# Optimization experiments

Measured on AMD Instinct MI355X. Metric: run time of the kernel, lower is better.

## Reference

```python
import jax, jax.numpy as jnp
import numpy as np

HEADS = 8
DIM_HEAD = 64


def setup_inputs() -> dict:
    key = jax.random.key(0)
    k1, k2, k3 = jax.random.split(key, 3)
    dim_in = 256
    hidden = HEADS * DIM_HEAD  # 512
    x = jax.random.normal(k1, (2, dim_in, 64, 64), dtype=jnp.float32)
    # 1x1 conv weights stored as [out_ch, in_ch]
    w_qkv = jax.random.normal(k2, (3 * hidden, dim_in), dtype=jnp.float32) * (1.0 / np.sqrt(dim_in))
    w_out = jax.random.normal(k3, (dim_in, hidden), dtype=jnp.float32) * (1.0 / np.sqrt(hidden))
    b_out = jnp.zeros((dim_in,), dtype=jnp.float32)
    return {"x": x, "w_qkv": w_qkv, "w_out": w_out, "b_out": b_out}


def reference(x, w_qkv, w_out, b_out):
    b, c, H, W = x.shape
    S = H * W
    scale = 1.0 / np.sqrt(DIM_HEAD)
    # 1x1 conv == per-pixel linear projection
    qkv = jnp.einsum('bcxy,oc->boxy', x, w_qkv)  # [b, 3*hidden, H, W]
    q, k, v = jnp.split(qkv, 3, axis=1)
    # 'b (h c) x y -> b h c (x y)'
    def to_heads(z):
        return z.reshape(b, HEADS, DIM_HEAD, S)
    q = to_heads(q) * scale
    k = to_heads(k)
    v = to_heads(v)
    sim = jnp.einsum('bhdi,bhdj->bhij', q, k)  # [b, h, S, S]
    sim = sim - jax.lax.stop_gradient(jnp.max(sim, axis=-1, keepdims=True))
    attn = jax.nn.softmax(sim, axis=-1)
    out = jnp.einsum('bhij,bhdj->bhid', attn, v)  # [b, h, S, d]
    # 'b h (x y) d -> b (h d) x y'
    out = out.transpose(0, 1, 3, 2).reshape(b, HEADS * DIM_HEAD, H, W)
    return jnp.einsum('bcxy,oc->boxy', out, w_out) + b_out[None, :, None, None]
```

## Files before the change

kernel.cpp:

```cpp
#include <hip/hip_runtime.h>
#include <cmath>

#define S_TOT 4096
#define CIN   256
#define HID   512
#define NHEAD 8
#define DIMH  64

typedef __attribute__((ext_vector_type(8))) short bf16x8;
typedef __attribute__((ext_vector_type(4))) float f32x4;
typedef __attribute__((address_space(1))) const void gv_t;
typedef __attribute__((address_space(3))) void lv_t;

__device__ __forceinline__ ushort f2bf(float f) {
    union { float f; unsigned u; } v; v.f = f;
    unsigned r = (v.u + 0x7FFFu + ((v.u >> 16) & 1u)) >> 16;
    return (ushort)r;
}

__device__ __forceinline__ float exp2_fast(float x) {
    float r; asm("v_exp_f32 %0, %1" : "=v"(r) : "v"(x)); return r;
}

__device__ __forceinline__ unsigned cvt_pk_bf16(float lo, float hi) {
    unsigned r; asm("v_cvt_pk_bf16_f32 %0, %1, %2" : "=v"(r) : "v"(lo), "v"(hi)); return r;
}

#define QSCALE 0.18033688011112042f

__global__ __launch_bounds__(256)
void cast_f32_bf16(const float* __restrict__ in, ushort* __restrict__ out, long n) {
    long i = ((long)blockIdx.x * 256 + threadIdx.x) * 4;
    if (i < n) {
        float4 v = *(const float4*)&in[i];
        ushort4 p;
        p.x = f2bf(v.x); p.y = f2bf(v.y); p.z = f2bf(v.z); p.w = f2bf(v.w);
        *(ushort4*)&out[i] = p;
    }
}

__global__ __launch_bounds__(256)
void transpose_cast_x(const float* __restrict__ x, ushort* __restrict__ xt) {
    __shared__ float tb[64][65];
    const int t = threadIdx.x;
    const int s0 = blockIdx.x * 64, c0 = blockIdx.y * 64;
    const long xb = (long)blockIdx.z * CIN * S_TOT;
    #pragma unroll
    for (int i = 0; i < 16; ++i) {
        int idx = t + i * 256;
        int c = idx >> 6, s = idx & 63;
        tb[c][s] = x[xb + (long)(c0 + c) * S_TOT + s0 + s];
    }
    __syncthreads();
    const long ob = (long)blockIdx.z * S_TOT * CIN;
    const int s = t >> 2, cq = (t & 3) * 16;
    #pragma unroll
    for (int j = 0; j < 4; ++j) {
        ushort4 pk;
        pk.x = f2bf(tb[cq + j * 4 + 0][s]);
        pk.y = f2bf(tb[cq + j * 4 + 1][s]);
        pk.z = f2bf(tb[cq + j * 4 + 2][s]);
        pk.w = f2bf(tb[cq + j * 4 + 3][s]);
        *(ushort4*)&xt[ob + (long)(s0 + s) * CIN + c0 + cq + j * 4] = pk;
    }
}

template<int MODE>
__global__ __launch_bounds__(256)
void gemm_mfma_kernel(const ushort* __restrict__ Ag, const ushort* __restrict__ Bg,
                      void* __restrict__ outp, const float* __restrict__ bias,
                      int Kdim, long strideA, long strideB) {
    __shared__ __attribute__((aligned(16))) ushort Abuf[128 * 64];
    __shared__ __attribute__((aligned(16))) ushort Bbuf[128 * 64];
    const int t = threadIdx.x, lane = t & 63;
    const int l15 = lane & 15, g = lane >> 4;
    const int wid = t >> 6, wr = wid >> 1, wc = wid & 1;
    const int bz = blockIdx.z;
    const int am0 = blockIdx.y * 128, bn0 = blockIdx.x * 128;
    Ag += (long)bz * strideA;
    Bg += (long)bz * strideB;

    f32x4 acc[4][4];
    #pragma unroll
    for (int i = 0; i < 4; ++i)
        #pragma unroll
        for (int j = 0; j < 4; ++j)
            acc[i][j] = (f32x4){0.f, 0.f, 0.f, 0.f};

    for (int k0 = 0; k0 < Kdim; k0 += 64) {
        __syncthreads();
        #pragma unroll
        for (int i = 0; i < 4; ++i) {
            const int chunk = t + i * 256;
            const int row = chunk >> 3, sl = chunk & 7;
            const ushort* srcA = Ag + (long)(am0 + row) * Kdim + k0 + ((sl ^ (row & 7)) << 3);
            __builtin_amdgcn_global_load_lds((gv_t*)srcA,
                (lv_t*)((char*)Abuf + (i * 256 + (t & ~63)) * 16), 16, 0, 0);
            const ushort* srcB = Bg + (long)(bn0 + row) * Kdim + k0 + ((sl ^ (row & 7)) << 3);
            __builtin_amdgcn_global_load_lds((gv_t*)srcB,
                (lv_t*)((char*)Bbuf + (i * 256 + (t & ~63)) * 16), 16, 0, 0);
        }
        asm volatile("s_waitcnt vmcnt(0)" ::: "memory");
        __syncthreads();

        bf16x8 bfr[4][2];
        #pragma unroll
        for (int fn = 0; fn < 4; ++fn) {
            const int row = wc * 64 + fn * 16 + l15;
            #pragma unroll
            for (int hf = 0; hf < 2; ++hf)
                bfr[fn][hf] = *(const bf16x8*)((const char*)Bbuf + row * 128
                                + (((hf * 4 + g) ^ (row & 7)) << 4));
        }
        #pragma unroll
        for (int fm = 0; fm < 4; ++fm) {
            const int row = wr * 64 + fm * 16 + l15;
            const bf16x8 a0 = *(const bf16x8*)((const char*)Abuf + row * 128
                                + (((g) ^ (row & 7)) << 4));
            const bf16x8 a1 = *(const bf16x8*)((const char*)Abuf + row * 128
                                + (((4 + g) ^ (row & 7)) << 4));
            #pragma unroll
            for (int fn = 0; fn < 4; ++fn) {
                acc[fm][fn] = __builtin_amdgcn_mfma_f32_16x16x32_bf16(a0, bfr[fn][0], acc[fm][fn], 0, 0, 0);
                acc[fm][fn] = __builtin_amdgcn_mfma_f32_16x16x32_bf16(a1, bfr[fn][1], acc[fm][fn], 0, 0, 0);
            }
        }
    }

    #pragma unroll
    for (int fm = 0; fm < 4; ++fm)
        #pragma unroll
        for (int fn = 0; fn < 4; ++fn)
            #pragma unroll
            for (int r = 0; r < 4; ++r) {
                const int ar = am0 + wr * 64 + fm * 16 + g * 4 + r;
                const int bc = bn0 + wc * 64 + fn * 16 + l15;
                if (MODE == 0) {
                    const int which = bc >> 9, h = (bc >> 6) & 7, d = bc & 63;
                    const float scl = (which == 0) ? QSCALE : 1.0f;
                    ushort* O = (ushort*)outp;
                    O[(long)which * 4194304 + (((long)(bz * NHEAD + h)) * S_TOT + ar) * DIMH + d]
                        = f2bf(acc[fm][fn][r] * scl);
                } else if (MODE == 1) {
                    const int h = ar >> 6, d = ar & 63;
                    const int j = bc & 63;
                    const int pj = ((j >> 5) << 5) | (((j >> 2) & 3) << 3)
                                 | (((j >> 4) & 1) << 2) | (j & 3);
                    const int pc = (bc & ~63) | pj;
                    ushort* O = (ushort*)outp;
                    O[(((long)(bz * NHEAD + h)) * DIMH + d) * S_TOT + pc] = f2bf(acc[fm][fn][r]);
                } else {
                    float* O = (float*)outp;
                    O[((long)bz * CIN + ar) * S_TOT + bc] = acc[fm][fn][r] + bias[ar];
                }
            }
}

__global__ __launch_bounds__(512)
void attn_mfma_kernel(const ushort* __restrict__ qg, const ushort* __restrict__ kg,
                      const ushort* __restrict__ vg, ushort* __restrict__ aout) {
    __shared__ __attribute__((aligned(16))) ushort kbuf[2][64 * 64];
    __shared__ __attribute__((aligned(16))) ushort vbuf[2][64 * 64];

    const int t = threadIdx.x;
    const int lane = t & 63, wid = t >> 6;
    const int l15 = lane & 15, g = lane >> 4;
    const int h = blockIdx.y, b = blockIdx.z;
    const int bh = b * NHEAD + h;
    const int qrow0 = blockIdx.x * 128 + wid * 16;

    const ushort* qp = qg + ((long)bh * S_TOT + qrow0 + l15) * DIMH + g * 8;
    const bf16x8 qf0 = *(const bf16x8*)qp;
    const bf16x8 qf1 = *(const bf16x8*)(qp + 32);

    f32x4 oacc[4];
    #pragma unroll
    for (int f = 0; f < 4; ++f) oacc[f] = (f32x4){0.f, 0.f, 0.f, 0.f};
    float mrun = -3e38f, lrun = 0.f;

    const long kg_base = (long)bh * S_TOT * DIMH;
    const long vg_base = (long)bh * DIMH * S_TOT;
    const int sl = lane & 7, sr = lane >> 3;
    const int swz = sl ^ sr;

    auto STAGE = [&](int buf, long key0) {
        const int row = wid * 8 + sr;
        char* kdst = (char*)(&kbuf[buf][0]) + wid * 1024;
        char* vdst = (char*)(&vbuf[buf][0]) + wid * 1024;
        const char* srcK = (const char*)(kg + kg_base + (key0 + row) * DIMH) + swz * 16;
        __builtin_amdgcn_global_load_lds((gv_t*)srcK, (lv_t*)kdst, 16, 0, 0);
        const char* srcV = (const char*)(vg + vg_base + (long)row * S_TOT + key0) + swz * 16;
        __builtin_amdgcn_global_load_lds((gv_t*)srcV, (lv_t*)vdst, 16, 0, 0);
    };

    STAGE(0, 0);
    asm volatile("s_waitcnt vmcnt(0)" ::: "memory");
    __syncthreads();

    for (int kt0 = 0; kt0 < S_TOT / 64; ++kt0) {
        const int cur = kt0 & 1;
        if (kt0 + 1 < S_TOT / 64) STAGE(cur ^ 1, (long)(kt0 + 1) * 64);

        const char* kb_ = (const char*)(&kbuf[cur][0]);
        const char* vb_ = (const char*)(&vbuf[cur][0]);

        f32x4 sacc[4];
        __builtin_amdgcn_s_setprio(1);
        #pragma unroll
        for (int kb = 0; kb < 4; ++kb) {
            const int krow = kb * 16 + l15, ks = krow & 7;
            const bf16x8 kf0 = *(const bf16x8*)(kb_ + krow * 128 + ((g ^ ks) << 4));
            const bf16x8 kf1 = *(const bf16x8*)(kb_ + krow * 128 + (((4 + g) ^ ks) << 4));
            sacc[kb] = (f32x4){0.f, 0.f, 0.f, 0.f};
            sacc[kb] = __builtin_amdgcn_mfma_f32_16x16x32_bf16(kf0, qf0, sacc[kb], 0, 0, 0);
            sacc[kb] = __builtin_amdgcn_mfma_f32_16x16x32_bf16(kf1, qf1, sacc[kb], 0, 0, 0);
        }
        __builtin_amdgcn_s_setprio(0);

        float tmax = fmaxf(fmaxf(sacc[0][0], sacc[0][1]), fmaxf(sacc[0][2], sacc[0][3]));
        #pragma unroll
        for (int kb = 1; kb < 4; ++kb)
            tmax = fmaxf(tmax, fmaxf(fmaxf(sacc[kb][0], sacc[kb][1]),
                                     fmaxf(sacc[kb][2], sacc[kb][3])));

        if (__any(tmax > mrun + 8.0f)) {
            float tm = fmaxf(tmax, __shfl_xor(tmax, 16, 64));
            tm = fmaxf(tm, __shfl_xor(tm, 32, 64));
            const float mn = fmaxf(mrun, tm);
            const float al = exp2_fast(mrun - mn);
            lrun *= al;
            #pragma unroll
            for (int r = 0; r < 4; ++r) {
                const float alg = __shfl(al, g * 4 + r, 64);
                #pragma unroll
                for (int f = 0; f < 4; ++f) oacc[f][r] *= alg;
            }
            mrun = mn;
        }

        union { unsigned u[8]; bf16x8 v[2]; } pw;
        #pragma unroll
        for (int kb = 0; kb < 4; ++kb) {
            const float p0 = exp2_fast(sacc[kb][0] - mrun);
            const float p1 = exp2_fast(sacc[kb][1] - mrun);
            const float p2 = exp2_fast(sacc[kb][2] - mrun);
            const float p3 = exp2_fast(sacc[kb][3] - mrun);
            lrun += (p0 + p1) + (p2 + p3);
            pw.u[kb * 2]     = cvt_pk_bf16(p0, p1);
            pw.u[kb * 2 + 1] = cvt_pk_bf16(p2, p3);
        }

        __builtin_amdgcn_s_setprio(1);
        #pragma unroll
        for (int ks = 0; ks < 2; ++ks) {
            #pragma unroll
            for (int f = 0; f < 4; ++f) {
                const int vrow = f * 16 + l15;
                const bf16x8 vf = *(const bf16x8*)(vb_ + vrow * 128
                                    + (((ks * 4 + g) ^ (vrow & 7)) << 4));
                oacc[f] = __builtin_amdgcn_mfma_f32_16x16x32_bf16(pw.v[ks], vf, oacc[f], 0, 0, 0);
            }
        }
        __builtin_amdgcn_s_setprio(0);

        asm volatile("s_waitcnt vmcnt(0)" ::: "memory");
        __syncthreads();
    }

    lrun += __shfl_xor(lrun, 16, 64);
    lrun += __shfl_xor(lrun, 32, 64);
    #pragma unroll
    for (int r = 0; r < 4; ++r) {
        const float inv = 1.0f / __shfl(lrun, g * 4 + r, 64);
        const long srow = (long)b * S_TOT + qrow0 + g * 4 + r;
        #pragma unroll
        for (int f = 0; f < 4; ++f)
            aout[srow * HID + h * 64 + f * 16 + l15] = f2bf(oacc[f][r] * inv);
    }
}

extern "C" void kernel_launch(void* const* d_in, const int* in_sizes, int n_in,
                              void* d_out, int out_size, void* d_ws, size_t ws_size,
                              hipStream_t stream) {
    const float* x     = (const float*)d_in[0];
    const float* w_qkv = (const float*)d_in[1];
    const float* w_out = (const float*)d_in[2];
    const float* b_out = (const float*)d_in[3];
    float* out = (float*)d_out;

    const long PERQKV = (long)2 * NHEAD * S_TOT * DIMH;
    ushort* qws = (ushort*)d_ws;
    ushort* kws = qws + PERQKV;
    ushort* vws = kws + PERQKV;
    ushort* xt  = vws + PERQKV;
    ushort* wqb = xt + (long)2 * S_TOT * CIN;
    ushort* wob = wqb + (long)3 * HID * CIN;
    ushort* awb = wob + (long)CIN * HID;

    cast_f32_bf16<<<dim3((3 * HID * CIN / 4 + 255) / 256), 256, 0, stream>>>(
        w_qkv, wqb, (long)3 * HID * CIN);
    cast_f32_bf16<<<dim3((CIN * HID / 4 + 255) / 256), 256, 0, stream>>>(
        w_out, wob, (long)CIN * HID);
    transpose_cast_x<<<dim3(S_TOT / 64, CIN / 64, 2), 256, 0, stream>>>(x, xt);

    gemm_mfma_kernel<0><<<dim3(1024 / 128, S_TOT / 128, 2), 256, 0, stream>>>(
        xt, wqb, qws, nullptr, CIN, (long)S_TOT * CIN, 0L);
    gemm_mfma_kernel<1><<<dim3(S_TOT / 128, 512 / 128, 2), 256, 0, stream>>>(
        wqb + (long)1024 * CIN, xt, vws, nullptr, CIN, 0L, (long)S_TOT * CIN);

    attn_mfma_kernel<<<dim3(S_TOT / 128, NHEAD, 2), 512, 0, stream>>>(qws, kws, vws, awb);

    gemm_mfma_kernel<2><<<dim3(S_TOT / 128, CIN / 128, 2), 256, 0, stream>>>(
        wob, awb, out, b_out, HID, 0L, (long)S_TOT * HID);
}
```

Baseline: 135.0 us.

## Switch attention to 32x32x16 MFMA tiles with 32 query rows per wave

The attention kernel moves from 16x16x32 MFMA to 32x32x16 MFMA. Each wave now owns 32 query rows, and each block uses 4 waves of 256 threads with two blocks per CU. The running max is folded into the QK accumulator as a bias initialiser, which removes the per-element subtraction before exp. The P fragments are rearranged with cross-lane shuffles, so the V-layout permutation in the projection GEMM is dropped. The aim is fewer MFMA instructions and LDS reads per tile, paid for with more registers and extra shuffle traffic.

```diff
diff --git a/kernel.cpp b/kernel.cpp
--- a/kernel.cpp
+++ b/kernel.cpp
@@ -9,6 +9,7 @@
 
 typedef __attribute__((ext_vector_type(8))) short bf16x8;
 typedef __attribute__((ext_vector_type(4))) float f32x4;
+typedef __attribute__((ext_vector_type(16))) float f32x16;
 typedef __attribute__((address_space(1))) const void gv_t;
 typedef __attribute__((address_space(3))) void lv_t;
 
@@ -143,12 +144,8 @@
                         = f2bf(acc[fm][fn][r] * scl);
                 } else if (MODE == 1) {
                     const int h = ar >> 6, d = ar & 63;
-                    const int j = bc & 63;
-                    const int pj = ((j >> 5) << 5) | (((j >> 2) & 3) << 3)
-                                 | (((j >> 4) & 1) << 2) | (j & 3);
-                    const int pc = (bc & ~63) | pj;
                     ushort* O = (ushort*)outp;
-                    O[(((long)(bz * NHEAD + h)) * DIMH + d) * S_TOT + pc] = f2bf(acc[fm][fn][r]);
+                    O[(((long)(bz * NHEAD + h)) * DIMH + d) * S_TOT + bc] = f2bf(acc[fm][fn][r]);
                 } else {
                     float* O = (float*)outp;
                     O[((long)bz * CIN + ar) * S_TOT + bc] = acc[fm][fn][r] + bias[ar];
@@ -156,7 +153,34 @@
             }
 }
 
-__global__ __launch_bounds__(512)
+#define MKPF(SV, PFA, PFB) do {                                               \
+    const float e0 = exp2_fast(SV[0]),  e1 = exp2_fast(SV[1]);               \
+    const float e2 = exp2_fast(SV[2]),  e3 = exp2_fast(SV[3]);               \
+    const float e4 = exp2_fast(SV[4]),  e5 = exp2_fast(SV[5]);               \
+    const float e6 = exp2_fast(SV[6]),  e7 = exp2_fast(SV[7]);               \
+    const float e8 = exp2_fast(SV[8]),  e9 = exp2_fast(SV[9]);               \
+    const float ea = exp2_fast(SV[10]), eb = exp2_fast(SV[11]);              \
+    const float ec = exp2_fast(SV[12]), ed = exp2_fast(SV[13]);              \
+    const float ee = exp2_fast(SV[14]), ef = exp2_fast(SV[15]);              \
+    lrun += (((e0+e1)+(e2+e3)) + ((e4+e5)+(e6+e7)))                          \
+          + (((e8+e9)+(ea+eb)) + ((ec+ed)+(ee+ef)));                         \
+    const unsigned x0 = cvt_pk_bf16(e0,e1), x1 = cvt_pk_bf16(e2,e3);         \
+    const unsigned x2 = cvt_pk_bf16(e4,e5), x3 = cvt_pk_bf16(e6,e7);         \
+    const unsigned y0 = cvt_pk_bf16(e8,e9), y1 = cvt_pk_bf16(ea,eb);         \
+    const unsigned y2 = cvt_pk_bf16(ec,ed), y3 = cvt_pk_bf16(ee,ef);         \
+    const unsigned sx0 = __shfl_xor((int)x0,32,64), sx1 = __shfl_xor((int)x1,32,64); \
+    const unsigned sx2 = __shfl_xor((int)x2,32,64), sx3 = __shfl_xor((int)x3,32,64); \
+    const unsigned sy0 = __shfl_xor((int)y0,32,64), sy1 = __shfl_xor((int)y1,32,64); \
+    const unsigned sy2 = __shfl_xor((int)y2,32,64), sy3 = __shfl_xor((int)y3,32,64); \
+    union { unsigned u[4]; bf16x8 v; } A_, B_;                               \
+    A_.u[0] = h ? sx2 : x0;  A_.u[1] = h ? sx3 : x1;                         \
+    A_.u[2] = h ? x2  : sx0; A_.u[3] = h ? x3  : sx1;                        \
+    B_.u[0] = h ? sy2 : y0;  B_.u[1] = h ? sy3 : y1;                         \
+    B_.u[2] = h ? y2  : sy0; B_.u[3] = h ? y3  : sy1;                        \
+    PFA = A_.v; PFB = B_.v;                                                  \
+} while (0)
+
+__global__ __launch_bounds__(256, 2)
 void attn_mfma_kernel(const ushort* __restrict__ qg, const ushort* __restrict__ kg,
                       const ushort* __restrict__ vg, ushort* __restrict__ aout) {
     __shared__ __attribute__((aligned(16))) ushort kbuf[2][64 * 64];
@@ -164,19 +188,20 @@
 
     const int t = threadIdx.x;
     const int lane = t & 63, wid = t >> 6;
-    const int l15 = lane & 15, g = lane >> 4;
-    const int h = blockIdx.y, b = blockIdx.z;
-    const int bh = b * NHEAD + h;
-    const int qrow0 = blockIdx.x * 128 + wid * 16;
-
-    const ushort* qp = qg + ((long)bh * S_TOT + qrow0 + l15) * DIMH + g * 8;
-    const bf16x8 qf0 = *(const bf16x8*)qp;
-    const bf16x8 qf1 = *(const bf16x8*)(qp + 32);
-
-    f32x4 oacc[4];
-    #pragma unroll
-    for (int f = 0; f < 4; ++f) oacc[f] = (f32x4){0.f, 0.f, 0.f, 0.f};
-    float mrun = -3e38f, lrun = 0.f;
+    const int l31 = lane & 31, h = lane >> 5;
+    const int sw7 = l31 & 7;
+    const int head = blockIdx.y, b = blockIdx.z;
+    const int bh = b * NHEAD + head;
+    const int qrow0 = blockIdx.x * 128 + wid * 32;
+
+    const ushort* qp = qg + ((long)bh * S_TOT + qrow0 + l31) * DIMH + h * 8;
+    bf16x8 qfr[4];
+    #pragma unroll
+    for (int ds = 0; ds < 4; ++ds) qfr[ds] = *(const bf16x8*)(qp + ds * 16);
+
+    f32x16 oacc0 = {}, oacc1 = {};
+    f32x16 bias16 = {};
+    float nmr = 0.f, lrun = 0.f;
 
     const long kg_base = (long)bh * S_TOT * DIMH;
     const long vg_base = (long)bh * DIMH * S_TOT;
@@ -184,13 +209,16 @@
     const int swz = sl ^ sr;
 
     auto STAGE = [&](int buf, long key0) {
-        const int row = wid * 8 + sr;
-        char* kdst = (char*)(&kbuf[buf][0]) + wid * 1024;
-        char* vdst = (char*)(&vbuf[buf][0]) + wid * 1024;
-        const char* srcK = (const char*)(kg + kg_base + (key0 + row) * DIMH) + swz * 16;
-        __builtin_amdgcn_global_load_lds((gv_t*)srcK, (lv_t*)kdst, 16, 0, 0);
-        const char* srcV = (const char*)(vg + vg_base + (long)row * S_TOT + key0) + swz * 16;
-        __builtin_amdgcn_global_load_lds((gv_t*)srcV, (lv_t*)vdst, 16, 0, 0);
+        #pragma unroll
+        for (int c = 0; c < 2; ++c) {
+            const int row = wid * 16 + c * 8 + sr;
+            char* kdst = (char*)(&kbuf[buf][0]) + wid * 2048 + c * 1024;
+            char* vdst = (char*)(&vbuf[buf][0]) + wid * 2048 + c * 1024;
+            const char* srcK = (const char*)(kg + kg_base + (key0 + row) * DIMH) + swz * 16;
+            __builtin_amdgcn_global_load_lds((gv_t*)srcK, (lv_t*)kdst, 16, 0, 0);
+            const char* srcV = (const char*)(vg + vg_base + (long)row * S_TOT + key0) + swz * 16;
+            __builtin_amdgcn_global_load_lds((gv_t*)srcV, (lv_t*)vdst, 16, 0, 0);
+        }
     };
 
     STAGE(0, 0);
@@ -204,62 +232,77 @@
         const char* kb_ = (const char*)(&kbuf[cur][0]);
         const char* vb_ = (const char*)(&vbuf[cur][0]);
 
-        f32x4 sacc[4];
+        f32x16 s0, s1;
         __builtin_amdgcn_s_setprio(1);
-        #pragma unroll
-        for (int kb = 0; kb < 4; ++kb) {
-            const int krow = kb * 16 + l15, ks = krow & 7;
-            const bf16x8 kf0 = *(const bf16x8*)(kb_ + krow * 128 + ((g ^ ks) << 4));
-            const bf16x8 kf1 = *(const bf16x8*)(kb_ + krow * 128 + (((4 + g) ^ ks) << 4));
-            sacc[kb] = (f32x4){0.f, 0.f, 0.f, 0.f};
-            sacc[kb] = __builtin_amdgcn_mfma_f32_16x16x32_bf16(kf0, qf0, sacc[kb], 0, 0, 0);
-            sacc[kb] = __builtin_amdgcn_mfma_f32_16x16x32_bf16(kf1, qf1, sacc[kb], 0, 0, 0);
+        {
+            const bf16x8 kf0 = *(const bf16x8*)(kb_ + l31 * 128 + ((h ^ sw7) << 4));
+            const bf16x8 kf1 = *(const bf16x8*)(kb_ + 4096 + l31 * 128 + ((h ^ sw7) << 4));
+            s0 = __builtin_amdgcn_mfma_f32_32x32x16_bf16(kf0, qfr[0], bias16, 0, 0, 0);
+            s1 = __builtin_amdgcn_mfma_f32_32x32x16_bf16(kf1, qfr[0], bias16, 0, 0, 0);
+        }
+        #pragma unroll
+        for (int ds = 1; ds < 4; ++ds) {
+            const bf16x8 kf0 = *(const bf16x8*)(kb_ + l31 * 128 + (((2 * ds + h) ^ sw7) << 4));
+            const bf16x8 kf1 = *(const bf16x8*)(kb_ + 4096 + l31 * 128 + (((2 * ds + h) ^ sw7) << 4));
+            s0 = __builtin_amdgcn_mfma_f32_32x32x16_bf16(kf0, qfr[ds], s0, 0, 0, 0);
+            s1 = __builtin_amdgcn_mfma_f32_32x32x16_bf16(kf1, qfr[ds], s1, 0, 0, 0);
         }
         __builtin_amdgcn_s_setprio(0);
 
-        float tmax = fmaxf(fmaxf(sacc[0][0], sacc[0][1]), fmaxf(sacc[0][2], sacc[0][3]));
-        #pragma unroll
-        for (int kb = 1; kb < 4; ++kb)
-            tmax = fmaxf(tmax, fmaxf(fmaxf(sacc[kb][0], sacc[kb][1]),
-                                     fmaxf(sacc[kb][2], sacc[kb][3])));
-
-        if (__any(tmax > mrun + 8.0f)) {
-            float tm = fmaxf(tmax, __shfl_xor(tmax, 16, 64));
-            tm = fmaxf(tm, __shfl_xor(tm, 32, 64));
-            const float mn = fmaxf(mrun, tm);
-            const float al = exp2_fast(mrun - mn);
+        float m0, m1;
+        {
+            float a0 = fmaxf(fmaxf(s0[0], s0[1]), fmaxf(s0[2], s0[3]));
+            float a1 = fmaxf(fmaxf(s0[4], s0[5]), fmaxf(s0[6], s0[7]));
+            float a2 = fmaxf(fmaxf(s0[8], s0[9]), fmaxf(s0[10], s0[11]));
+            float a3 = fmaxf(fmaxf(s0[12], s0[13]), fmaxf(s0[14], s0[15]));
+            m0 = fmaxf(fmaxf(a0, a1), fmaxf(a2, a3));
+            float b0 = fmaxf(fmaxf(s1[0], s1[1]), fmaxf(s1[2], s1[3]));
+            float b1 = fmaxf(fmaxf(s1[4], s1[5]), fmaxf(s1[6], s1[7]));
+            float b2 = fmaxf(fmaxf(s1[8], s1[9]), fmaxf(s1[10], s1[11]));
+            float b3 = fmaxf(fmaxf(s1[12], s1[13]), fmaxf(s1[14], s1[15]));
+            m1 = fmaxf(fmaxf(b0, b1), fmaxf(b2, b3));
+        }
+        const float tmax = fmaxf(m0, m1);
+
+        if (__any(tmax > 8.0f)) {
+            const float tm = fmaxf(fmaxf(tmax, __shfl_xor(tmax, 32, 64)), 0.0f);
+            const float al = exp2_fast(-tm);
             lrun *= al;
             #pragma unroll
-            for (int r = 0; r < 4; ++r) {
-                const float alg = __shfl(al, g * 4 + r, 64);
-                #pragma unroll
-                for (int f = 0; f < 4; ++f) oacc[f][r] *= alg;
+            for (int r = 0; r < 16; ++r) {
+                const float alg = __shfl(al, (r & 3) + 8 * (r >> 2) + 4 * h, 64);
+                oacc0[r] *= alg;
+                oacc1[r] *= alg;
             }
-            mrun = mn;
-        }
-
-        union { unsigned u[8]; bf16x8 v[2]; } pw;
-        #pragma unroll
-        for (int kb = 0; kb < 4; ++kb) {
-            const float p0 = exp2_fast(sacc[kb][0] - mrun);
-            const float p1 = exp2_fast(sacc[kb][1] - mrun);
-            const float p2 = exp2_fast(sacc[kb][2] - mrun);
-            const float p3 = exp2_fast(sacc[kb][3] - mrun);
-            lrun += (p0 + p1) + (p2 + p3);
-            pw.u[kb * 2]     = cvt_pk_bf16(p0, p1);
-            pw.u[kb * 2 + 1] = cvt_pk_bf16(p2, p3);
-        }
+            #pragma unroll
+            for (int r = 0; r < 16; ++r) { s0[r] -= tm; s1[r] -= tm; }
+            nmr -= tm;
+            #pragma unroll
+            for (int r = 0; r < 16; ++r) bias16[r] = nmr;
+        }
+
+        bf16x8 pf0, pf1, pf2, pf3;
+        MKPF(s0, pf0, pf1);
+        MKPF(s1, pf2, pf3);
 
         __builtin_amdgcn_s_setprio(1);
-        #pragma unroll
-        for (int ks = 0; ks < 2; ++ks) {
-            #pragma unroll
-            for (int f = 0; f < 4; ++f) {
-                const int vrow = f * 16 + l15;
-                const bf16x8 vf = *(const bf16x8*)(vb_ + vrow * 128
-                                    + (((ks * 4 + g) ^ (vrow & 7)) << 4));
-                oacc[f] = __builtin_amdgcn_mfma_f32_16x16x32_bf16(pw.v[ks], vf, oacc[f], 0, 0, 0);
-            }
+        {
+            const bf16x8 vf00 = *(const bf16x8*)(vb_ + l31 * 128 + ((h ^ sw7) << 4));
+            const bf16x8 vf01 = *(const bf16x8*)(vb_ + 4096 + l31 * 128 + ((h ^ sw7) << 4));
+            oacc0 = __builtin_amdgcn_mfma_f32_32x32x16_bf16(pf0, vf00, oacc0, 0, 0, 0);
+            oacc1 = __builtin_amdgcn_mfma_f32_32x32x16_bf16(pf0, vf01, oacc1, 0, 0, 0);
+            const bf16x8 vf10 = *(const bf16x8*)(vb_ + l31 * 128 + (((2 + h) ^ sw7) << 4));
+            const bf16x8 vf11 = *(const bf16x8*)(vb_ + 4096 + l31 * 128 + (((2 + h) ^ sw7) << 4));
+            oacc0 = __builtin_amdgcn_mfma_f32_32x32x16_bf16(pf1, vf10, oacc0, 0, 0, 0);
+            oacc1 = __builtin_amdgcn_mfma_f32_32x32x16_bf16(pf1, vf11, oacc1, 0, 0, 0);
+            const bf16x8 vf20 = *(const bf16x8*)(vb_ + l31 * 128 + (((4 + h) ^ sw7) << 4));
+            const bf16x8 vf21 = *(const bf16x8*)(vb_ + 4096 + l31 * 128 + (((4 + h) ^ sw7) << 4));
+            oacc0 = __builtin_amdgcn_mfma_f32_32x32x16_bf16(pf2, vf20, oacc0, 0, 0, 0);
+            oacc1 = __builtin_amdgcn_mfma_f32_32x32x16_bf16(pf2, vf21, oacc1, 0, 0, 0);
+            const bf16x8 vf30 = *(const bf16x8*)(vb_ + l31 * 128 + (((6 + h) ^ sw7) << 4));
+            const bf16x8 vf31 = *(const bf16x8*)(vb_ + 4096 + l31 * 128 + (((6 + h) ^ sw7) << 4));
+            oacc0 = __builtin_amdgcn_mfma_f32_32x32x16_bf16(pf3, vf30, oacc0, 0, 0, 0);
+            oacc1 = __builtin_amdgcn_mfma_f32_32x32x16_bf16(pf3, vf31, oacc1, 0, 0, 0);
         }
         __builtin_amdgcn_s_setprio(0);
 
@@ -267,15 +310,15 @@
         __syncthreads();
     }
 
-    lrun += __shfl_xor(lrun, 16, 64);
     lrun += __shfl_xor(lrun, 32, 64);
-    #pragma unroll
-    for (int r = 0; r < 4; ++r) {
-        const float inv = 1.0f / __shfl(lrun, g * 4 + r, 64);
-        const long srow = (long)b * S_TOT + qrow0 + g * 4 + r;
-        #pragma unroll
-        for (int f = 0; f < 4; ++f)
-            aout[srow * HID + h * 64 + f * 16 + l15] = f2bf(oacc[f][r] * inv);
+    const float inv = 1.0f / lrun;
+    #pragma unroll
+    for (int r = 0; r < 16; ++r) {
+        const int q = (r & 3) + 8 * (r >> 2) + 4 * h;
+        const float invr = __shfl(inv, q, 64);
+        const long srow = (long)b * S_TOT + qrow0 + q;
+        aout[srow * HID + head * 64 + l31]      = f2bf(oacc0[r] * invr);
+        aout[srow * HID + head * 64 + 32 + l31] = f2bf(oacc1[r] * invr);
     }
 }
 
@@ -308,7 +351,7 @@
     gemm_mfma_kernel<1><<<dim3(S_TOT / 128, 512 / 128, 2), 256, 0, stream>>>(
         wqb + (long)1024 * CIN, xt, vws, nullptr, CIN, 0L, (long)S_TOT * CIN);
 
-    attn_mfma_kernel<<<dim3(S_TOT / 128, NHEAD, 2), 512, 0, stream>>>(qws, kws, vws, awb);
+    attn_mfma_kernel<<<dim3(S_TOT / 128, NHEAD, 2), 256, 0, stream>>>(qws, kws, vws, awb);
 
     gemm_mfma_kernel<2><<<dim3(S_TOT / 128, CIN / 128, 2), 256, 0, stream>>>(
         wob, awb, out, b_out, HID, 0L, (long)S_TOT * HID);
```

Result: slower. 163.6 us (+21.1%).
